# Performance work log

Hardware: AMD Instinct MI355X
Metric: run time of the kernel (lower is better)

## Reference

```python
import jax, jax.numpy as jnp
import numpy as np

HEADS = 8


def setup_inputs() -> dict:
    key = jax.random.key(0)
    ks = jax.random.split(key, 7)
    B, C, H, W = 8, 512, 64, 64
    K, MEM = 64, 512
    s = 0.02
    return {
        "x": jax.random.normal(ks[0], (B, C, H, W), dtype=jnp.float32),
        "Ft": jax.random.normal(ks[1], (B, K, MEM), dtype=jnp.float32),
        "Wq": jax.random.normal(ks[2], (C, C), dtype=jnp.float32) * s,
        "Wk": jax.random.normal(ks[3], (C, MEM), dtype=jnp.float32) * s,
        "Wv": jax.random.normal(ks[4], (C, MEM), dtype=jnp.float32) * s,
        "Wp": jax.random.normal(ks[5], (C, C), dtype=jnp.float32) * s,
        "bp": jax.random.normal(ks[6], (C,), dtype=jnp.float32) * s,
    }


def reference(x, Ft, Wq, Wk, Wv, Wp, bp):
    B, C, H, W = x.shape
    h = HEADS
    d = C // h
    N = H * W
    # 1x1 conv query projection: (out_c, in_c) applied over spatial dims
    q = jnp.einsum('oc,bchw->bohw', Wq, x).reshape(B, h, d, N)
    q = jnp.transpose(q, (0, 1, 3, 2))                      # [B,h,N,d]
    # Linear K/V on memory tokens: Ft [B,K,MEM] @ W^T -> [B,K,C]
    k = (Ft @ Wk.T).reshape(B, -1, h, d).transpose(0, 2, 1, 3)  # [B,h,K,d]
    v = (Ft @ Wv.T).reshape(B, -1, h, d).transpose(0, 2, 1, 3)  # [B,h,K,d]
    attn = jnp.einsum('bhnc,bhkc->bhnk', q, k) / jnp.sqrt(jnp.float32(d))
    attn = jax.nn.softmax(attn, axis=-1)
    out = jnp.einsum('bhnk,bhkc->bhnc', attn, v)            # [B,h,N,d]
    out = jnp.transpose(out, (0, 1, 3, 2)).reshape(B, C, H, W)
    out = jnp.einsum('oc,bchw->bohw', Wp, out) + bp[None, :, None, None]
    return x + out
```

## Files before the change

kernel.cpp:

```cpp
#include <hip/hip_runtime.h>
#include <cstdint>
#include <cstddef>

#define BATCH 8
#define CDIM  512
#define NPIX  4096
#define NHEAD 8
#define DH    64
#define KTOK  64
#define MEM   512

#define BK    64

typedef __attribute__((ext_vector_type(8))) short          bf8;
typedef __attribute__((ext_vector_type(4))) float          f4;
typedef __attribute__((ext_vector_type(4))) unsigned short us4;

__device__ __forceinline__ unsigned short f2bf(float f){
  union { float f; unsigned int u; } x; x.f = f;
  unsigned int r = (x.u + 0x7fffu + ((x.u >> 16) & 1u)) >> 16;
  return (unsigned short)r;
}

__device__ __forceinline__ void gld_lds16(const unsigned short* g, unsigned short* lds){
  __builtin_amdgcn_global_load_lds((const __attribute__((address_space(1))) unsigned int*)g,
                                   (__attribute__((address_space(3))) unsigned int*)lds, 16, 0, 0);
}

__global__ __launch_bounds__(256) void wconv(const float* __restrict__ wq, const float* __restrict__ wp,
                                             unsigned short* __restrict__ wqb, unsigned short* __restrict__ wpb){
  int i = (blockIdx.x * 256 + threadIdx.x) * 4;
  float4 a = *(const float4*)(wq + i);
  us4 pa = { f2bf(a.x), f2bf(a.y), f2bf(a.z), f2bf(a.w) };
  *(us4*)(wqb + i) = pa;
  float4 b = *(const float4*)(wp + i);
  us4 pb = { f2bf(b.x), f2bf(b.y), f2bf(b.z), f2bf(b.w) };
  *(us4*)(wpb + i) = pb;
}

__global__ __launch_bounds__(256) void xtrans(const float* __restrict__ x, unsigned short* __restrict__ xb){
  __shared__ __align__(16) unsigned short t[64 * 68];
  int tid = threadIdx.x;
  int n0 = blockIdx.x * 64, c0 = blockIdx.y * 64, b = blockIdx.z;
  const float* xp = x + ((size_t)(b * CDIM + c0)) * NPIX + n0;
#pragma unroll
  for (int it = 0; it < 4; ++it){
    int idx = it * 1024 + tid * 4;
    int cc = idx >> 6, nn = idx & 63;
    float4 v = *(const float4*)(xp + (size_t)cc * NPIX + nn);
    us4 pk = { f2bf(v.x), f2bf(v.y), f2bf(v.z), f2bf(v.w) };
    *(us4*)&t[cc * 68 + nn] = pk;
  }
  __syncthreads();
  unsigned short* op = xb + ((size_t)(b * NPIX + n0)) * CDIM + c0;
#pragma unroll
  for (int it = 0; it < 4; ++it){
    int idx = it * 1024 + tid * 4;
    int nn = idx >> 6, c4 = idx & 63;
    us4 pk = { t[(c4 + 0) * 68 + nn], t[(c4 + 1) * 68 + nn],
               t[(c4 + 2) * 68 + nn], t[(c4 + 3) * 68 + nn] };
    *(us4*)(op + (size_t)nn * CDIM + c4) = pk;
  }
}

__global__ __launch_bounds__(256) void kvproj(const float* __restrict__ Ft, const float* __restrict__ Wk,
                                              const float* __restrict__ Wv, unsigned short* __restrict__ kb,
                                              unsigned short* __restrict__ vt){
  __shared__ float ft[8][MEM];
  int tid = threadIdx.x;
  int cg = blockIdx.x, kk0 = blockIdx.y * 8, b = blockIdx.z;
  const float* fp = Ft + ((size_t)(b * KTOK + kk0)) * MEM;
#pragma unroll
  for (int it = 0; it < 4; ++it){
    int idx = it * 1024 + tid * 4;
    int row = idx >> 9, m = idx & 511;
    *(float4*)&ft[row][m] = *(const float4*)(fp + (size_t)row * MEM + m);
  }
  __syncthreads();
  int kv = tid >> 7, cl = tid & 127;
  int c = cg * 128 + cl;
  const float* wrow = (kv ? Wv : Wk) + (size_t)c * MEM;
  float acc[8] = {0.f,0.f,0.f,0.f,0.f,0.f,0.f,0.f};
  for (int m = 0; m < MEM; m += 4){
    float4 wv4 = *(const float4*)(wrow + m);
#pragma unroll
    for (int kk = 0; kk < 8; ++kk){
      acc[kk] += wv4.x * ft[kk][m] + wv4.y * ft[kk][m+1] + wv4.z * ft[kk][m+2] + wv4.w * ft[kk][m+3];
    }
  }
  int h = c >> 6, dd = c & 63;
  if (kv == 0){
#pragma unroll
    for (int kk = 0; kk < 8; ++kk)
      kb[(((size_t)(b * NHEAD + h)) * KTOK + kk0 + kk) * DH + dd] = f2bf(acc[kk] * 0.125f);
  } else {
#pragma unroll
    for (int kk = 0; kk < 8; ++kk)
      vt[(((size_t)(b * NHEAD + h)) * DH + dd) * KTOK + kk0 + kk] = f2bf(acc[kk]);
  }
}

__global__ __launch_bounds__(256, 3) void qattn(const unsigned short* __restrict__ wqb,
                                                const unsigned short* __restrict__ xb,
                                                const unsigned short* __restrict__ kb,
                                                const unsigned short* __restrict__ vt,
                                                unsigned short* __restrict__ att){
  __shared__ __align__(16) unsigned short ab[16384];
  int tid = threadIdx.x;
  int w = tid >> 6, l = tid & 63;
  int lo = l & 15, hi = l >> 4;
  int n0 = blockIdx.x * 128, o0 = blockIdx.y * 128, b = blockIdx.z;
  int ol = (w >> 1) * 64, nl = (w & 1) * 64;

  f4 z = {0.f, 0.f, 0.f, 0.f};
  f4 accq[4][4];
#pragma unroll
  for (int i = 0; i < 4; ++i)
#pragma unroll
    for (int j = 0; j < 4; ++j) accq[i][j] = z;

  const int lrow = l >> 3;
  const int lcc  = (l & 7) ^ lrow;
  const unsigned short* asrc = wqb + ((size_t)(o0 + w * 8 + lrow)) * CDIM + lcc * 8;
  const unsigned short* bsrc = xb + ((size_t)(b * NPIX + n0 + w * 8 + lrow)) * CDIM + lcc * 8;

  for (int t = 0; t < 8; ++t){
    int kc = t * BK;
#pragma unroll
    for (int j = 0; j < 4; ++j){
      int g = j * 4 + w;
      gld_lds16(asrc + (size_t)j * 32 * CDIM + kc, &ab[g * 512]);
      gld_lds16(bsrc + (size_t)j * 32 * CDIM + kc, &ab[8192 + g * 512]);
    }
    __syncthreads();
#pragma unroll
    for (int ks = 0; ks < 2; ++ks){
      int cc = ks * 4 + hi;
      int sw = ((cc ^ (lo & 7)) << 3);
      bf8 af[4], bfr[4];
#pragma unroll
      for (int fi = 0; fi < 4; ++fi)
        af[fi] = *(const bf8*)&ab[(ol + fi * 16 + lo) * 64 + sw];
#pragma unroll
      for (int fj = 0; fj < 4; ++fj)
        bfr[fj] = *(const bf8*)&ab[8192 + (nl + fj * 16 + lo) * 64 + sw];
#pragma unroll
      for (int fi = 0; fi < 4; ++fi)
#pragma unroll
        for (int fj = 0; fj < 4; ++fj)
          accq[fi][fj] = __builtin_amdgcn_mfma_f32_16x16x32_bf16(af[fi], bfr[fj], accq[fi][fj], 0, 0, 0);
    }
    __syncthreads();
  }

  unsigned short* qt = &ab[w * 4096];
#pragma unroll
  for (int fi = 0; fi < 4; ++fi)
#pragma unroll
    for (int fj = 0; fj < 4; ++fj){
      f4 v = accq[fi][fj];
      us4 pk = { f2bf(v[0]), f2bf(v[1]), f2bf(v[2]), f2bf(v[3]) };
      int row = fj * 16 + lo;
      int col = fi * 16 + hi * 4;
      int cs  = (((col >> 3) ^ (row & 7)) << 3) | (col & 7);
      *(us4*)&qt[row * 64 + cs] = pk;
    }

  int head = blockIdx.y * 2 + (w >> 1);
  const unsigned short* kh = kb + ((size_t)(b * NHEAD + head)) * (KTOK * DH);
  f4 accs[4][4];
#pragma unroll
  for (int i = 0; i < 4; ++i)
#pragma unroll
    for (int j = 0; j < 4; ++j) accs[i][j] = z;
#pragma unroll
  for (int ks = 0; ks < 2; ++ks){
    int sw = (((ks * 4 + hi) ^ (lo & 7)) << 3);
    bf8 ka[4];
#pragma unroll
    for (int fi = 0; fi < 4; ++fi)
      ka[fi] = *(const bf8*)(kh + (fi * 16 + lo) * 64 + ks * 32 + hi * 8);
#pragma unroll
    for (int fj = 0; fj < 4; ++fj){
      bf8 qf = *(const bf8*)&qt[(fj * 16 + lo) * 64 + sw];
#pragma unroll
      for (int fi = 0; fi < 4; ++fi)
        accs[fi][fj] = __builtin_amdgcn_mfma_f32_16x16x32_bf16(ka[fi], qf, accs[fi][fj], 0, 0, 0);
    }
  }

#pragma unroll
  for (int fj = 0; fj < 4; ++fj){
    float mx = accs[0][fj][0];
#pragma unroll
    for (int fi = 0; fi < 4; ++fi)
#pragma unroll
      for (int r = 0; r < 4; ++r) mx = fmaxf(mx, accs[fi][fj][r]);
    mx = fmaxf(mx, __shfl_xor(mx, 16));
    mx = fmaxf(mx, __shfl_xor(mx, 32));
    float sm = 0.f;
#pragma unroll
    for (int fi = 0; fi < 4; ++fi)
#pragma unroll
      for (int r = 0; r < 4; ++r){
        float e = __expf(accs[fi][fj][r] - mx);
        accs[fi][fj][r] = e; sm += e;
      }
    sm += __shfl_xor(sm, 16);
    sm += __shfl_xor(sm, 32);
    float inv = 1.0f / sm;
#pragma unroll
    for (int fi = 0; fi < 4; ++fi){
      us4 pk = { f2bf(accs[fi][fj][0] * inv), f2bf(accs[fi][fj][1] * inv),
                 f2bf(accs[fi][fj][2] * inv), f2bf(accs[fi][fj][3] * inv) };
      int row = fj * 16 + lo;
      int col = fi * 16 + hi * 4;
      int cs  = (((col >> 3) ^ (row & 7)) << 3) | (col & 7);
      *(us4*)&qt[row * 64 + cs] = pk;
    }
  }

  const unsigned short* vh = vt + ((size_t)(b * NHEAD + head)) * (DH * KTOK);
  f4 acco[4][4];
#pragma unroll
  for (int i = 0; i < 4; ++i)
#pragma unroll
    for (int j = 0; j < 4; ++j) acco[i][j] = z;
#pragma unroll
  for (int ks = 0; ks < 2; ++ks){
    int sw = (((ks * 4 + hi) ^ (lo & 7)) << 3);
    bf8 va[4];
#pragma unroll
    for (int fi = 0; fi < 4; ++fi)
      va[fi] = *(const bf8*)(vh + (fi * 16 + lo) * 64 + ks * 32 + hi * 8);
#pragma unroll
    for (int fj = 0; fj < 4; ++fj){
      bf8 pf = *(const bf8*)&qt[(fj * 16 + lo) * 64 + sw];
#pragma unroll
      for (int fi = 0; fi < 4; ++fi)
        acco[fi][fj] = __builtin_amdgcn_mfma_f32_16x16x32_bf16(va[fi], pf, acco[fi][fj], 0, 0, 0);
    }
  }

  unsigned short* op = att + ((size_t)(b * NPIX + n0 + nl)) * CDIM + head * 64;
#pragma unroll
  for (int fi = 0; fi < 4; ++fi)
#pragma unroll
    for (int fj = 0; fj < 4; ++fj){
      f4 v = acco[fi][fj];
      us4 pk = { f2bf(v[0]), f2bf(v[1]), f2bf(v[2]), f2bf(v[3]) };
      *(us4*)(op + (size_t)(fj * 16 + lo) * CDIM + fi * 16 + hi * 4) = pk;
    }
}

__global__ __launch_bounds__(256, 3) void pproj(const unsigned short* __restrict__ wpb,
                                                const unsigned short* __restrict__ att,
                                                const float* __restrict__ x,
                                                const float* __restrict__ bpv,
                                                float* __restrict__ out){
  __shared__ __align__(16) unsigned short ab[16384];
  int tid = threadIdx.x;
  int w = tid >> 6, l = tid & 63;
  int lo = l & 15, hi = l >> 4;
  int n0 = blockIdx.x * 128, o0 = blockIdx.y * 128, b = blockIdx.z;
  int ol = (w >> 1) * 64, nl = (w & 1) * 64;

  f4 z = {0.f, 0.f, 0.f, 0.f};
  f4 acc[4][4];
#pragma unroll
  for (int i = 0; i < 4; ++i)
#pragma unroll
    for (int j = 0; j < 4; ++j) acc[i][j] = z;

  const int lrow = l >> 3;
  const int lcc  = (l & 7) ^ lrow;
  const unsigned short* asrc = wpb + ((size_t)(o0 + w * 8 + lrow)) * CDIM + lcc * 8;
  const unsigned short* bsrc = att + ((size_t)(b * NPIX + n0 + w * 8 + lrow)) * CDIM + lcc * 8;

  for (int t = 0; t < 8; ++t){
    int kc = t * BK;
#pragma unroll
    for (int j = 0; j < 4; ++j){
      int g = j * 4 + w;
      gld_lds16(asrc + (size_t)j * 32 * CDIM + kc, &ab[g * 512]);
      gld_lds16(bsrc + (size_t)j * 32 * CDIM + kc, &ab[8192 + g * 512]);
    }
    __syncthreads();
#pragma unroll
    for (int ks = 0; ks < 2; ++ks){
      int cc = ks * 4 + hi;
      int sw = ((cc ^ (lo & 7)) << 3);
      bf8 af[4], bfr[4];
#pragma unroll
      for (int fi = 0; fi < 4; ++fi)
        af[fi] = *(const bf8*)&ab[(ol + fi * 16 + lo) * 64 + sw];
#pragma unroll
      for (int fj = 0; fj < 4; ++fj)
        bfr[fj] = *(const bf8*)&ab[8192 + (nl + fj * 16 + lo) * 64 + sw];
#pragma unroll
      for (int fi = 0; fi < 4; ++fi)
#pragma unroll
        for (int fj = 0; fj < 4; ++fj)
          acc[fi][fj] = __builtin_amdgcn_mfma_f32_16x16x32_bf16(af[fi], bfr[fj], acc[fi][fj], 0, 0, 0);
    }
    __syncthreads();
  }

#pragma unroll
  for (int fi = 0; fi < 4; ++fi)
#pragma unroll
    for (int fj = 0; fj < 4; ++fj){
      int o = o0 + ol + fi * 16 + hi * 4;
      int n = n0 + nl + fj * 16 + lo;
#pragma unroll
      for (int r = 0; r < 4; ++r){
        size_t idx = ((size_t)(b * CDIM + o + r)) * NPIX + n;
        out[idx] = acc[fi][fj][r] + bpv[o + r] + x[idx];
      }
    }
}

extern "C" void kernel_launch(void* const* d_in, const int* in_sizes, int n_in,
                              void* d_out, int out_size, void* d_ws, size_t ws_size,
                              hipStream_t stream){
  const float* x  = (const float*)d_in[0];
  const float* Ft = (const float*)d_in[1];
  const float* Wq = (const float*)d_in[2];
  const float* Wk = (const float*)d_in[3];
  const float* Wv = (const float*)d_in[4];
  const float* Wp = (const float*)d_in[5];
  const float* bp = (const float*)d_in[6];
  float* out = (float*)d_out;

  char* ws = (char*)d_ws;
  unsigned short* wqb = (unsigned short*)(ws);
  unsigned short* wpb = (unsigned short*)(ws + 524288);
  unsigned short* xb  = (unsigned short*)(ws + 1048576);
  unsigned short* att = (unsigned short*)(ws + 1048576 + 33554432);
  unsigned short* kb  = (unsigned short*)(ws + 1048576 + 2ull * 33554432);
  unsigned short* vt  = (unsigned short*)(ws + 1048576 + 2ull * 33554432 + 524288);

  wconv<<<dim3(256), dim3(256), 0, stream>>>(Wq, Wp, wqb, wpb);
  xtrans<<<dim3(64, 8, 8), dim3(256), 0, stream>>>(x, xb);
  kvproj<<<dim3(4, 8, 8), dim3(256), 0, stream>>>(Ft, Wk, Wv, kb, vt);
  qattn<<<dim3(32, 4, 8), dim3(256), 0, stream>>>(wqb, xb, kb, vt, att);
  pproj<<<dim3(32, 4, 8), dim3(256), 0, stream>>>(wpb, att, x, bp, out);
}
```

Measured before the change: 115.7 us.

## Merge prep kernels and widen GEMM tiles to 256 pixels with direct weight loads

The three preprocessing kernels (weight conversion, x transpose to bf16, K/V projection) are merged into one launch that picks its role from the block index. This removes two launch gaps. The query and output projection GEMMs now use 512-thread blocks covering 128x256 tiles, so each x/att tile in LDS is shared by twice as many output columns. The weight operand is no longer staged in LDS and is read straight from global memory (L2) into registers. That cuts LDS traffic and halves the number of blocks, but weight loads are exposed to global latency and occupancy is lower.

```diff
diff --git a/kernel.cpp b/kernel.cpp
--- a/kernel.cpp
+++ b/kernel.cpp
@@ -10,8 +10,6 @@
 #define KTOK  64
 #define MEM   512
 
-#define BK    64
-
 typedef __attribute__((ext_vector_type(8))) short          bf8;
 typedef __attribute__((ext_vector_type(4))) float          f4;
 typedef __attribute__((ext_vector_type(4))) unsigned short us4;
@@ -27,90 +25,92 @@
                                    (__attribute__((address_space(3))) unsigned int*)lds, 16, 0, 0);
 }
 
-__global__ __launch_bounds__(256) void wconv(const float* __restrict__ wq, const float* __restrict__ wp,
-                                             unsigned short* __restrict__ wqb, unsigned short* __restrict__ wpb){
-  int i = (blockIdx.x * 256 + threadIdx.x) * 4;
-  float4 a = *(const float4*)(wq + i);
-  us4 pa = { f2bf(a.x), f2bf(a.y), f2bf(a.z), f2bf(a.w) };
-  *(us4*)(wqb + i) = pa;
-  float4 b = *(const float4*)(wp + i);
-  us4 pb = { f2bf(b.x), f2bf(b.y), f2bf(b.z), f2bf(b.w) };
-  *(us4*)(wpb + i) = pb;
-}
-
-__global__ __launch_bounds__(256) void xtrans(const float* __restrict__ x, unsigned short* __restrict__ xb){
-  __shared__ __align__(16) unsigned short t[64 * 68];
-  int tid = threadIdx.x;
-  int n0 = blockIdx.x * 64, c0 = blockIdx.y * 64, b = blockIdx.z;
-  const float* xp = x + ((size_t)(b * CDIM + c0)) * NPIX + n0;
-#pragma unroll
-  for (int it = 0; it < 4; ++it){
-    int idx = it * 1024 + tid * 4;
-    int cc = idx >> 6, nn = idx & 63;
-    float4 v = *(const float4*)(xp + (size_t)cc * NPIX + nn);
-    us4 pk = { f2bf(v.x), f2bf(v.y), f2bf(v.z), f2bf(v.w) };
-    *(us4*)&t[cc * 68 + nn] = pk;
-  }
-  __syncthreads();
-  unsigned short* op = xb + ((size_t)(b * NPIX + n0)) * CDIM + c0;
-#pragma unroll
-  for (int it = 0; it < 4; ++it){
-    int idx = it * 1024 + tid * 4;
-    int nn = idx >> 6, c4 = idx & 63;
-    us4 pk = { t[(c4 + 0) * 68 + nn], t[(c4 + 1) * 68 + nn],
-               t[(c4 + 2) * 68 + nn], t[(c4 + 3) * 68 + nn] };
-    *(us4*)(op + (size_t)nn * CDIM + c4) = pk;
-  }
-}
-
-__global__ __launch_bounds__(256) void kvproj(const float* __restrict__ Ft, const float* __restrict__ Wk,
-                                              const float* __restrict__ Wv, unsigned short* __restrict__ kb,
-                                              unsigned short* __restrict__ vt){
-  __shared__ float ft[8][MEM];
-  int tid = threadIdx.x;
-  int cg = blockIdx.x, kk0 = blockIdx.y * 8, b = blockIdx.z;
-  const float* fp = Ft + ((size_t)(b * KTOK + kk0)) * MEM;
-#pragma unroll
-  for (int it = 0; it < 4; ++it){
-    int idx = it * 1024 + tid * 4;
-    int row = idx >> 9, m = idx & 511;
-    *(float4*)&ft[row][m] = *(const float4*)(fp + (size_t)row * MEM + m);
-  }
-  __syncthreads();
-  int kv = tid >> 7, cl = tid & 127;
-  int c = cg * 128 + cl;
-  const float* wrow = (kv ? Wv : Wk) + (size_t)c * MEM;
-  float acc[8] = {0.f,0.f,0.f,0.f,0.f,0.f,0.f,0.f};
-  for (int m = 0; m < MEM; m += 4){
-    float4 wv4 = *(const float4*)(wrow + m);
-#pragma unroll
-    for (int kk = 0; kk < 8; ++kk){
-      acc[kk] += wv4.x * ft[kk][m] + wv4.y * ft[kk][m+1] + wv4.z * ft[kk][m+2] + wv4.w * ft[kk][m+3];
-    }
-  }
-  int h = c >> 6, dd = c & 63;
-  if (kv == 0){
-#pragma unroll
-    for (int kk = 0; kk < 8; ++kk)
-      kb[(((size_t)(b * NHEAD + h)) * KTOK + kk0 + kk) * DH + dd] = f2bf(acc[kk] * 0.125f);
+__global__ __launch_bounds__(256) void prep(const float* __restrict__ x, const float* __restrict__ Ft,
+                                            const float* __restrict__ Wq, const float* __restrict__ Wk,
+                                            const float* __restrict__ Wv, const float* __restrict__ Wp,
+                                            unsigned short* __restrict__ wqb, unsigned short* __restrict__ wpb,
+                                            unsigned short* __restrict__ xb, unsigned short* __restrict__ kb,
+                                            unsigned short* __restrict__ vt){
+  __shared__ __align__(16) unsigned char smem[16384];
+  int bid = blockIdx.x, tid = threadIdx.x;
+  if (bid < 4096){
+    unsigned short* t = (unsigned short*)smem;
+    int n0 = (bid & 63) * 64, c0 = ((bid >> 6) & 7) * 64, b = bid >> 9;
+    const float* xp = x + ((size_t)(b * CDIM + c0)) * NPIX + n0;
+#pragma unroll
+    for (int it = 0; it < 4; ++it){
+      int idx = it * 1024 + tid * 4;
+      int cc = idx >> 6, nn = idx & 63;
+      float4 v = *(const float4*)(xp + (size_t)cc * NPIX + nn);
+      us4 pk = { f2bf(v.x), f2bf(v.y), f2bf(v.z), f2bf(v.w) };
+      *(us4*)&t[cc * 68 + nn] = pk;
+    }
+    __syncthreads();
+    unsigned short* op = xb + ((size_t)(b * NPIX + n0)) * CDIM + c0;
+#pragma unroll
+    for (int it = 0; it < 4; ++it){
+      int idx = it * 1024 + tid * 4;
+      int nn = idx >> 6, c4 = idx & 63;
+      us4 pk = { t[(c4 + 0) * 68 + nn], t[(c4 + 1) * 68 + nn],
+                 t[(c4 + 2) * 68 + nn], t[(c4 + 3) * 68 + nn] };
+      *(us4*)(op + (size_t)nn * CDIM + c4) = pk;
+    }
+  } else if (bid < 4352){
+    int i = ((bid - 4096) * 256 + tid) * 4;
+    float4 a = *(const float4*)(Wq + i);
+    us4 pa = { f2bf(a.x), f2bf(a.y), f2bf(a.z), f2bf(a.w) };
+    *(us4*)(wqb + i) = pa;
+    float4 bq = *(const float4*)(Wp + i);
+    us4 pb = { f2bf(bq.x), f2bf(bq.y), f2bf(bq.z), f2bf(bq.w) };
+    *(us4*)(wpb + i) = pb;
   } else {
-#pragma unroll
-    for (int kk = 0; kk < 8; ++kk)
-      vt[(((size_t)(b * NHEAD + h)) * DH + dd) * KTOK + kk0 + kk] = f2bf(acc[kk]);
-  }
-}
-
-__global__ __launch_bounds__(256, 3) void qattn(const unsigned short* __restrict__ wqb,
+    float (*ft)[MEM] = (float(*)[MEM])smem;
+    int t2 = bid - 4352;
+    int cg = t2 & 3, kk0 = ((t2 >> 2) & 7) * 8, b = t2 >> 5;
+    const float* fp = Ft + ((size_t)(b * KTOK + kk0)) * MEM;
+#pragma unroll
+    for (int it = 0; it < 4; ++it){
+      int idx = it * 1024 + tid * 4;
+      int row = idx >> 9, m = idx & 511;
+      *(float4*)&ft[row][m] = *(const float4*)(fp + (size_t)row * MEM + m);
+    }
+    __syncthreads();
+    int kv = tid >> 7, cl = tid & 127;
+    int c = cg * 128 + cl;
+    const float* wrow = (kv ? Wv : Wk) + (size_t)c * MEM;
+    float acc[8] = {0.f,0.f,0.f,0.f,0.f,0.f,0.f,0.f};
+    for (int m = 0; m < MEM; m += 4){
+      float4 wv4 = *(const float4*)(wrow + m);
+#pragma unroll
+      for (int kk = 0; kk < 8; ++kk){
+        acc[kk] += wv4.x * ft[kk][m] + wv4.y * ft[kk][m+1] + wv4.z * ft[kk][m+2] + wv4.w * ft[kk][m+3];
+      }
+    }
+    int h = c >> 6, dd = c & 63;
+    if (kv == 0){
+#pragma unroll
+      for (int kk = 0; kk < 8; ++kk)
+        kb[(((size_t)(b * NHEAD + h)) * KTOK + kk0 + kk) * DH + dd] = f2bf(acc[kk] * 0.125f);
+    } else {
+#pragma unroll
+      for (int kk = 0; kk < 8; ++kk)
+        vt[(((size_t)(b * NHEAD + h)) * DH + dd) * KTOK + kk0 + kk] = f2bf(acc[kk]);
+    }
+  }
+}
+
+
+__global__ __launch_bounds__(512, 4) void qattn(const unsigned short* __restrict__ wqb,
                                                 const unsigned short* __restrict__ xb,
                                                 const unsigned short* __restrict__ kb,
                                                 const unsigned short* __restrict__ vt,
                                                 unsigned short* __restrict__ att){
-  __shared__ __align__(16) unsigned short ab[16384];
+  __shared__ __align__(16) unsigned short r0[32768];
   int tid = threadIdx.x;
   int w = tid >> 6, l = tid & 63;
   int lo = l & 15, hi = l >> 4;
-  int n0 = blockIdx.x * 128, o0 = blockIdx.y * 128, b = blockIdx.z;
-  int ol = (w >> 1) * 64, nl = (w & 1) * 64;
+  int n0 = blockIdx.x * 256, o0 = blockIdx.y * 128, b = blockIdx.z;
+  int ol = (w >> 2) * 64, nl = (w & 3) * 64;
 
   f4 z = {0.f, 0.f, 0.f, 0.f};
   f4 accq[4][4];
@@ -120,30 +120,26 @@
     for (int j = 0; j < 4; ++j) accq[i][j] = z;
 
   const int lrow = l >> 3;
-  const int lcc  = (l & 7) ^ lrow;
-  const unsigned short* asrc = wqb + ((size_t)(o0 + w * 8 + lrow)) * CDIM + lcc * 8;
-  const unsigned short* bsrc = xb + ((size_t)(b * NPIX + n0 + w * 8 + lrow)) * CDIM + lcc * 8;
+  const int lchk = (l & 7) ^ lrow;
+  const unsigned short* bS = xb + ((size_t)(b * NPIX) + n0 + w * 8 + lrow) * CDIM + lchk * 8;
+  const unsigned short* aW = wqb + (size_t)(o0 + ol + lo) * CDIM + hi * 8;
 
   for (int t = 0; t < 8; ++t){
-    int kc = t * BK;
-#pragma unroll
-    for (int j = 0; j < 4; ++j){
-      int g = j * 4 + w;
-      gld_lds16(asrc + (size_t)j * 32 * CDIM + kc, &ab[g * 512]);
-      gld_lds16(bsrc + (size_t)j * 32 * CDIM + kc, &ab[8192 + g * 512]);
-    }
+#pragma unroll
+    for (int j = 0; j < 4; ++j)
+      gld_lds16(bS + (size_t)j * 64 * CDIM + t * 64, &r0[(w + j * 8) * 512]);
     __syncthreads();
 #pragma unroll
     for (int ks = 0; ks < 2; ++ks){
-      int cc = ks * 4 + hi;
-      int sw = ((cc ^ (lo & 7)) << 3);
       bf8 af[4], bfr[4];
 #pragma unroll
       for (int fi = 0; fi < 4; ++fi)
-        af[fi] = *(const bf8*)&ab[(ol + fi * 16 + lo) * 64 + sw];
-#pragma unroll
-      for (int fj = 0; fj < 4; ++fj)
-        bfr[fj] = *(const bf8*)&ab[8192 + (nl + fj * 16 + lo) * 64 + sw];
+        af[fi] = *(const bf8*)(aW + (size_t)fi * 16 * CDIM + t * 64 + ks * 32);
+#pragma unroll
+      for (int fj = 0; fj < 4; ++fj){
+        int r = nl + fj * 16 + lo;
+        bfr[fj] = *(const bf8*)&r0[r * 64 + (((ks * 4 + hi) ^ (r & 7)) << 3)];
+      }
 #pragma unroll
       for (int fi = 0; fi < 4; ++fi)
 #pragma unroll
@@ -153,7 +149,7 @@
     __syncthreads();
   }
 
-  unsigned short* qt = &ab[w * 4096];
+  unsigned short* qt = &r0[w * 4096];
 #pragma unroll
   for (int fi = 0; fi < 4; ++fi)
 #pragma unroll
@@ -166,8 +162,8 @@
       *(us4*)&qt[row * 64 + cs] = pk;
     }
 
-  int head = blockIdx.y * 2 + (w >> 1);
-  const unsigned short* kh = kb + ((size_t)(b * NHEAD + head)) * (KTOK * DH);
+  int head = blockIdx.y * 2 + (w >> 2);
+  const unsigned short* kh = kb + (size_t)(b * NHEAD + head) * (KTOK * DH);
   f4 accs[4][4];
 #pragma unroll
   for (int i = 0; i < 4; ++i)
@@ -175,14 +171,13 @@
     for (int j = 0; j < 4; ++j) accs[i][j] = z;
 #pragma unroll
   for (int ks = 0; ks < 2; ++ks){
-    int sw = (((ks * 4 + hi) ^ (lo & 7)) << 3);
     bf8 ka[4];
 #pragma unroll
     for (int fi = 0; fi < 4; ++fi)
       ka[fi] = *(const bf8*)(kh + (fi * 16 + lo) * 64 + ks * 32 + hi * 8);
 #pragma unroll
     for (int fj = 0; fj < 4; ++fj){
-      bf8 qf = *(const bf8*)&qt[(fj * 16 + lo) * 64 + sw];
+      bf8 qf = *(const bf8*)&qt[(fj * 16 + lo) * 64 + (((ks * 4 + hi) ^ (lo & 7)) << 3)];
 #pragma unroll
       for (int fi = 0; fi < 4; ++fi)
         accs[fi][fj] = __builtin_amdgcn_mfma_f32_16x16x32_bf16(ka[fi], qf, accs[fi][fj], 0, 0, 0);
@@ -220,7 +215,7 @@
     }
   }
 
-  const unsigned short* vh = vt + ((size_t)(b * NHEAD + head)) * (DH * KTOK);
+  const unsigned short* vh = vt + (size_t)(b * NHEAD + head) * (DH * KTOK);
   f4 acco[4][4];
 #pragma unroll
   for (int i = 0; i < 4; ++i)
@@ -242,7 +237,7 @@
     }
   }
 
-  unsigned short* op = att + ((size_t)(b * NPIX + n0 + nl)) * CDIM + head * 64;
+  unsigned short* op = att + ((size_t)(b * NPIX) + n0 + nl) * CDIM + head * 64;
 #pragma unroll
   for (int fi = 0; fi < 4; ++fi)
 #pragma unroll
@@ -253,17 +248,17 @@
     }
 }
 
-__global__ __launch_bounds__(256, 3) void pproj(const unsigned short* __restrict__ wpb,
+__global__ __launch_bounds__(512, 4) void pproj(const unsigned short* __restrict__ wpb,
                                                 const unsigned short* __restrict__ att,
                                                 const float* __restrict__ x,
                                                 const float* __restrict__ bpv,
                                                 float* __restrict__ out){
-  __shared__ __align__(16) unsigned short ab[16384];
+  __shared__ __align__(16) unsigned short bb[16384];
   int tid = threadIdx.x;
   int w = tid >> 6, l = tid & 63;
   int lo = l & 15, hi = l >> 4;
-  int n0 = blockIdx.x * 128, o0 = blockIdx.y * 128, b = blockIdx.z;
-  int ol = (w >> 1) * 64, nl = (w & 1) * 64;
+  int n0 = blockIdx.x * 256, o0 = blockIdx.y * 128, b = blockIdx.z;
+  int ol = (w >> 2) * 64, nl = (w & 3) * 64;
 
   f4 z = {0.f, 0.f, 0.f, 0.f};
   f4 acc[4][4];
@@ -273,30 +268,26 @@
     for (int j = 0; j < 4; ++j) acc[i][j] = z;
 
   const int lrow = l >> 3;
-  const int lcc  = (l & 7) ^ lrow;
-  const unsigned short* asrc = wpb + ((size_t)(o0 + w * 8 + lrow)) * CDIM + lcc * 8;
-  const unsigned short* bsrc = att + ((size_t)(b * NPIX + n0 + w * 8 + lrow)) * CDIM + lcc * 8;
+  const int lchk = (l & 7) ^ lrow;
+  const unsigned short* bS = att + ((size_t)(b * NPIX) + n0 + w * 8 + lrow) * CDIM + lchk * 8;
+  const unsigned short* aW = wpb + (size_t)(o0 + ol + lo) * CDIM + hi * 8;
 
   for (int t = 0; t < 8; ++t){
-    int kc = t * BK;
-#pragma unroll
-    for (int j = 0; j < 4; ++j){
-      int g = j * 4 + w;
-      gld_lds16(asrc + (size_t)j * 32 * CDIM + kc, &ab[g * 512]);
-      gld_lds16(bsrc + (size_t)j * 32 * CDIM + kc, &ab[8192 + g * 512]);
-    }
+#pragma unroll
+    for (int j = 0; j < 4; ++j)
+      gld_lds16(bS + (size_t)j * 64 * CDIM + t * 64, &bb[(w + j * 8) * 512]);
     __syncthreads();
 #pragma unroll
     for (int ks = 0; ks < 2; ++ks){
-      int cc = ks * 4 + hi;
-      int sw = ((cc ^ (lo & 7)) << 3);
       bf8 af[4], bfr[4];
 #pragma unroll
       for (int fi = 0; fi < 4; ++fi)
-        af[fi] = *(const bf8*)&ab[(ol + fi * 16 + lo) * 64 + sw];
-#pragma unroll
-      for (int fj = 0; fj < 4; ++fj)
-        bfr[fj] = *(const bf8*)&ab[8192 + (nl + fj * 16 + lo) * 64 + sw];
+        af[fi] = *(const bf8*)(aW + (size_t)fi * 16 * CDIM + t * 64 + ks * 32);
+#pragma unroll
+      for (int fj = 0; fj < 4; ++fj){
+        int r = nl + fj * 16 + lo;
+        bfr[fj] = *(const bf8*)&bb[r * 64 + (((ks * 4 + hi) ^ (r & 7)) << 3)];
+      }
 #pragma unroll
       for (int fi = 0; fi < 4; ++fi)
 #pragma unroll
@@ -340,9 +331,7 @@
   unsigned short* kb  = (unsigned short*)(ws + 1048576 + 2ull * 33554432);
   unsigned short* vt  = (unsigned short*)(ws + 1048576 + 2ull * 33554432 + 524288);
 
-  wconv<<<dim3(256), dim3(256), 0, stream>>>(Wq, Wp, wqb, wpb);
-  xtrans<<<dim3(64, 8, 8), dim3(256), 0, stream>>>(x, xb);
-  kvproj<<<dim3(4, 8, 8), dim3(256), 0, stream>>>(Ft, Wk, Wv, kb, vt);
-  qattn<<<dim3(32, 4, 8), dim3(256), 0, stream>>>(wqb, xb, kb, vt, att);
-  pproj<<<dim3(32, 4, 8), dim3(256), 0, stream>>>(wpb, att, x, bp, out);
-}
+  prep<<<dim3(4608), dim3(256), 0, stream>>>(x, Ft, Wq, Wk, Wv, Wp, wqb, wpb, xb, kb, vt);
+  qattn<<<dim3(16, 4, 8), dim3(512), 0, stream>>>(wqb, xb, kb, vt, att);
+  pproj<<<dim3(16, 4, 8), dim3(512), 0, stream>>>(wpb, att, x, bp, out);
+}
```

After: 174.6 us. 1.51x slower.
